# Kernel tuning notes

Hardware: AMD Instinct MI355X
Metric: run time of the kernel (lower is better)

## Reference

```python
import jax, jax.numpy as jnp
import numpy as np

N_SAMPLES = 2 ** 15  # 32768
NYQUIST = 22050.0 / 2.0
MIN_FREQ = 40.0 / NYQUIST
MAX_FREQ = 4000.0 / NYQUIST
FREQ_RANGE = MAX_FREQ - MIN_FREQ


def interp_linear(x, out_size):
    """torch F.interpolate(mode='linear', align_corners=False) along last axis."""
    in_size = x.shape[-1]
    scale = in_size / out_size
    coords = (jnp.arange(out_size, dtype=x.dtype) + 0.5) * scale - 0.5
    coords = jnp.clip(coords, 0.0, in_size - 1)
    lo = jnp.floor(coords).astype(jnp.int32)
    hi = jnp.minimum(lo + 1, in_size - 1)
    w = coords - lo.astype(x.dtype)
    return x[..., lo] * (1.0 - w) + x[..., hi] * w


def translate(pair, shift, scale):
    # angle of complex(pair[:,:,0], pair[:,:,1]) / pi, then affine
    angle = jnp.arctan2(pair[:, :, 1, :], pair[:, :, 0, :]) / np.pi
    return shift + angle * scale


def setup_inputs() -> dict:
    key = jax.random.key(0)
    k1, k2 = jax.random.split(key)
    x = jax.random.normal(k1, (16, 8, 10, 128), dtype=jnp.float32)
    noise = jax.random.normal(k2, (16, 8, N_SAMPLES), dtype=jnp.float32)
    return {"x": x, "noise": noise}


def reference(x, noise):
    # x: (batch, n_osc, 10, time_ctrl); noise: (batch, n_osc, N_SAMPLES)
    basic = x[:, :, 0:2, :]
    amp = jnp.sqrt(jnp.sum(basic * basic, axis=2))            # (b, o, t)
    amp = interp_linear(amp, N_SAMPLES)                       # (b, o, N)

    f0 = translate(basic, MIN_FREQ, FREQ_RANGE)               # control-rate
    mix = interp_linear(translate(x[:, :, 2:4, :], 1.0, 0.5), N_SAMPLES)
    harm_amp = amp * mix
    noise_amp = amp * (1.0 - mix)

    noise_std = translate(x[:, :, 4:6, :], MIN_FREQ, FREQ_RANGE)
    mod_factor = translate(x[:, :, 6:8, :], 0.25, 4.75)
    b = translate(x[:, :, 8:10, :], 0.1, 9.9)

    # band_filtered_noise: narrowband noise as a frequency-jittered sine
    f0_fr = interp_linear(f0, N_SAMPLES)
    std_fr = interp_linear(noise_std, N_SAMPLES)
    bfn = jnp.sin(jnp.cumsum(f0_fr + noise * std_fr, axis=-1))
    noise_sig = noise_amp * bfn

    mod_factor = interp_linear(mod_factor, N_SAMPLES)
    b = interp_linear(b, N_SAMPLES)
    mod = b * jnp.sin(jnp.cumsum(mod_factor, axis=-1))
    sig = harm_amp * jnp.sin(jnp.cumsum(f0_fr, axis=-1) + mod)

    mixed = noise_sig + sig                                   # (b, o, N)
    return jnp.mean(mixed, axis=1, keepdims=True)             # (b, 1, N)
```

## Files before the change

kernel.cpp:

```cpp
#include <hip/hip_runtime.h>
#include <math.h>

#define NS     32768
#define NB     128
#define CELL   16
#define CPB    32
#define PART   (CELL * CPB)
#define NPARTS (NS / PART)
#define TPB    256
#define NBATCH 16
#define GRID   (NBATCH * NPARTS)

__device__ __forceinline__ float sinr(float x) {
    return __builtin_amdgcn_sinf(x - rintf(x));
}

__device__ __forceinline__ void seg_params(int i, int& lo, int& hi,
                                           double& w0, double& wst) {
    if (i < 128)            { lo = 0;   hi = 1;   w0 = 0.0; wst = 0.0; }
    else if (i >= NS - 128) { lo = 127; hi = 127; w0 = 0.0; wst = 0.0; }
    else {
        lo = (i - 128) >> 8;  hi = lo + 1;
        int off = (i - 128) & 255;
        w0 = (off + 0.5) * (1.0 / 256.0);
        wst = 1.0 / 256.0;
    }
}

__device__ __forceinline__ double bin_value(const float* xs, int q, int j) {
    const double PI_    = 3.14159265358979323846;
    const double INV2PI = 0.15915494309189533576888376337251;
    const double MINF   = 40.0 / 11025.0;
    const double FRNG   = (4000.0 - 40.0) / 11025.0;
    if (q == 0) {
        double a0 = (double)xs[j], a1 = (double)xs[NB + j];
        return sqrt(a0 * a0 + a1 * a1);
    }
    double ang = atan2((double)xs[(2 * q - 1) * NB + j],
                       (double)xs[(2 * q - 2) * NB + j]) / PI_;
    double sh, sc;
    if      (q == 1) { sh = MINF; sc = FRNG; }
    else if (q == 2) { sh = 1.0;  sc = 0.5;  }
    else if (q == 3) { sh = MINF; sc = FRNG; }
    else if (q == 4) { sh = 0.25; sc = 4.75; }
    else             { sh = 0.1;  sc = 9.9;  }
    double v = sh + ang * sc;
    if (q != 2) v *= INV2PI;
    return v;
}

__device__ __forceinline__ void cell_totals(
        const float4* nn, double f0L, double dF0, double stL, double dSt,
        double mfL, double dMf, double w0, double wst,
        double& t1, double& t3, double& t2) {
    float4 A0 = nn[0], A1 = nn[1], A2 = nn[2], A3 = nn[3];
    float nf[CELL] = {A0.x, A0.y, A0.z, A0.w, A1.x, A1.y, A1.z, A1.w,
                      A2.x, A2.y, A2.z, A2.w, A3.x, A3.y, A3.z, A3.w};
    double S0 = 0.0, S1 = 0.0;
    #pragma unroll
    for (int j = 0; j < CELL; ++j) {
        S0 += (double)nf[j];
        S1 += (double)j * (double)nf[j];
    }
    double sw = 16.0 * w0 + 120.0 * wst;
    t3 = 16.0 * f0L + dF0 * sw;
    t2 = 16.0 * mfL + dMf * sw;
    t1 = t3 + stL * S0 + dSt * (w0 * S0 + wst * S1);
}

__global__ __launch_bounds__(TPB, 4)
void span_kernel(const float* __restrict__ xg, const float* __restrict__ ng,
                 double* __restrict__ wspan) {
    __shared__ double binsA[8][3][4];
    __shared__ double wtot[4][8][3];

    int bx = blockIdx.x, b = bx >> 6, p = bx & (NPARTS - 1);
    int tid = threadIdx.x, lane = tid & 63, wid = tid >> 6;
    int h = tid & 7, c = tid >> 3;
    int P = p * PART;
    int b0 = (P - 128) >> 8; if (b0 < 0) b0 = 0;

    int s  = (b << 3) + h;
    int i0 = P + c * CELL;
    const float4* nn = reinterpret_cast<const float4*>(ng + (size_t)s * NS + i0);

    if (tid < 96) {
        int j = tid & 3, r = (tid >> 2) % 3, h2 = tid / 12;
        int q = (r == 0) ? 1 : (r == 1) ? 3 : 4;
        const float* xs = xg + (size_t)((b << 3) + h2) * 10 * NB;
        binsA[h2][r][j] = bin_value(xs, q, min(b0 + j, NB - 1));
    }
    __syncthreads();

    int lo, hi; double w0, wst;
    seg_params(i0, lo, hi, w0, wst);
    int jL = lo - b0, jH = hi - b0;
    double f0L = binsA[h][0][jL], dF0 = binsA[h][0][jH] - f0L;
    double stL = binsA[h][1][jL], dSt = binsA[h][1][jH] - stL;
    double mfL = binsA[h][2][jL], dMf = binsA[h][2][jH] - mfL;

    double t1, t3, t2;
    cell_totals(nn, f0L, dF0, stL, dSt, mfL, dMf, w0, wst, t1, t3, t2);

    double v1 = t1, v3 = t3, v2 = t2;
    #pragma unroll
    for (int d = 8; d < 64; d <<= 1) {
        double u1 = __shfl_up(v1, d);
        double u3 = __shfl_up(v3, d);
        double u2 = __shfl_up(v2, d);
        if (lane >= d) { v1 += u1; v3 += u3; v2 += u2; }
    }
    if (lane >= 56) { wtot[wid][h][0] = v1; wtot[wid][h][1] = v3; wtot[wid][h][2] = v2; }
    __syncthreads();
    if (tid < 24) {
        int hh = tid & 7, k = tid >> 3;
        double t = wtot[0][hh][k] + wtot[1][hh][k] + wtot[2][hh][k] + wtot[3][hh][k];
        wspan[((size_t)(((b << 3) + hh) * NPARTS) + p) * 3 + k] = t;
    }
}

__global__ __launch_bounds__(TPB, 4)
void fm2_kernel(const float* __restrict__ xg, const float* __restrict__ ng,
                const double* __restrict__ wspan, float* __restrict__ out) {
    __shared__ double binsA[8][3][4];
    __shared__ float  binsB[8][6][4];
    __shared__ double wtot[4][8][3];
    __shared__ double pref[8][3];

    int bx = blockIdx.x, b = bx >> 6, p = bx & (NPARTS - 1);
    int tid = threadIdx.x, lane = tid & 63, wid = tid >> 6;
    int h = tid & 7, c = tid >> 3;
    int P = p * PART;
    int b0 = (P - 128) >> 8; if (b0 < 0) b0 = 0;

    int s  = (b << 3) + h;
    int i0 = P + c * CELL;
    const float4* nn = reinterpret_cast<const float4*>(ng + (size_t)s * NS + i0);
    float4 A0 = nn[0], A1 = nn[1], A2 = nn[2], A3 = nn[3];

    if (tid < 192) {
        int j = tid & 3, q = (tid >> 2) % 6, h2 = tid / 24;
        const float* xs = xg + (size_t)((b << 3) + h2) * 10 * NB;
        double v = bin_value(xs, q, min(b0 + j, NB - 1));
        binsB[h2][q][j] = (float)v;
        if      (q == 1) binsA[h2][0][j] = v;
        else if (q == 3) binsA[h2][1][j] = v;
        else if (q == 4) binsA[h2][2][j] = v;
    } else if (tid < 216) {
        int t2 = tid - 192, hh = t2 & 7, k = t2 >> 3;
        const double* sp = wspan + ((size_t)(((b << 3) + hh) * NPARTS)) * 3 + k;
        double acc = 0.0;
        for (int q2 = 0; q2 < p; ++q2) acc += sp[q2 * 3];
        pref[hh][k] = acc;
    }
    __syncthreads();

    int lo, hi; double w0, wst;
    seg_params(i0, lo, hi, w0, wst);
    int jL = lo - b0, jH = hi - b0;
    double f0L = binsA[h][0][jL], dF0 = binsA[h][0][jH] - f0L;
    double stL = binsA[h][1][jL], dSt = binsA[h][1][jH] - stL;
    double mfL = binsA[h][2][jL], dMf = binsA[h][2][jH] - mfL;

    double t1, t3, t2;
    cell_totals(nn, f0L, dF0, stL, dSt, mfL, dMf, w0, wst, t1, t3, t2);

    double v1 = t1, v3 = t3, v2 = t2;
    #pragma unroll
    for (int d = 8; d < 64; d <<= 1) {
        double u1 = __shfl_up(v1, d);
        double u3 = __shfl_up(v3, d);
        double u2 = __shfl_up(v2, d);
        if (lane >= d) { v1 += u1; v3 += u3; v2 += u2; }
    }
    if (lane >= 56) { wtot[wid][h][0] = v1; wtot[wid][h][1] = v3; wtot[wid][h][2] = v2; }
    __syncthreads();
    double b1 = 0.0, b3 = 0.0, b2 = 0.0;
    #pragma unroll
    for (int k = 0; k < 3; ++k)
        if (wid > k) { b1 += wtot[k][h][0]; b3 += wtot[k][h][1]; b2 += wtot[k][h][2]; }

    double a1 = pref[h][0] + b1 + (v1 - t1);
    double a3 = pref[h][1] + b3 + (v3 - t3);
    double a2 = pref[h][2] + b2 + (v2 - t2);
    float fr1 = (float)(a1 - rint(a1));
    float fr3 = (float)(a3 - rint(a3));
    float fr2 = (float)(a2 - rint(a2));

    float amL = binsB[h][0][jL], dAm = binsB[h][0][jH] - amL;
    float g0L = binsB[h][1][jL], gF0 = binsB[h][1][jH] - g0L;
    float mxL = binsB[h][2][jL], dMx = binsB[h][2][jH] - mxL;
    float gsL = binsB[h][3][jL], gSt = binsB[h][3][jH] - gsL;
    float gmL = binsB[h][4][jL], gMf = binsB[h][4][jH] - gmL;
    float bbL = binsB[h][5][jL], dBb = binsB[h][5][jH] - bbL;
    float w0f = (float)w0, wsf = (float)wst;

    float nf[CELL] = {A0.x, A0.y, A0.z, A0.w, A1.x, A1.y, A1.z, A1.w,
                      A2.x, A2.y, A2.z, A2.w, A3.x, A3.y, A3.z, A3.w};
    float arr[CELL];
    float d1 = 0.f, d2 = 0.f, d3 = 0.f;
    #pragma unroll
    for (int j = 0; j < CELL; ++j) {
        float wf  = fmaf((float)j, wsf, w0f);
        float f0v = fmaf(wf, gF0, g0L);
        float stv = fmaf(wf, gSt, gsL);
        float mfv = fmaf(wf, gMf, gmL);
        d3 += f0v;
        d1 += fmaf(nf[j], stv, f0v);
        d2 += mfv;
        float ampv = fmaf(wf, dAm, amL);
        float mixv = fmaf(wf, dMx, mxL);
        float bv   = fmaf(wf, dBb, bbL);
        float s2 = sinr(fr2 + d2);
        float s1 = sinr(fr1 + d1);
        float s3 = sinr(fmaf(bv, s2, fr3 + d3));
        float harm = ampv * mixv;
        arr[j] = fmaf(harm, s3, (ampv - harm) * s1);
    }

    #pragma unroll
    for (int m = 1; m <= 4; m <<= 1) {
        #pragma unroll
        for (int j = 0; j < CELL; ++j) arr[j] += __shfl_xor(arr[j], m);
    }
    if (h == 0) {
        float4* op = reinterpret_cast<float4*>(out + (size_t)b * NS + i0);
        #pragma unroll
        for (int j4 = 0; j4 < 4; ++j4)
            op[j4] = make_float4(arr[j4 * 4 + 0] * 0.125f, arr[j4 * 4 + 1] * 0.125f,
                                 arr[j4 * 4 + 2] * 0.125f, arr[j4 * 4 + 3] * 0.125f);
    }
}

extern "C" void kernel_launch(void* const* d_in, const int* in_sizes, int n_in,
                              void* d_out, int out_size, void* d_ws, size_t ws_size,
                              hipStream_t stream) {
    const float* x     = (const float*)d_in[0];
    const float* noise = (const float*)d_in[1];
    float* out = (float*)d_out;
    double* wspan = (double*)d_ws;
    span_kernel<<<GRID, TPB, 0, stream>>>(x, noise, wspan);
    fm2_kernel<<<GRID, TPB, 0, stream>>>(x, noise, wspan, out);
}
```

Measured before the change: 85.42 us.

## Split scan into three kernels with stored per-cell prefixes and precomputed bins

The pipeline is restructured into three stages. The first computes per-cell exclusive prefixes and per-span totals and writes both to workspace, using a 32-lane shuffle scan per oscillator so no LDS cross-wave reduction is needed. A small fix kernel then scans the span totals and precomputes every control-bin value. The final kernel reads these instead of redoing the noise summation, the serial span-prefix loop and the bin evaluation. The cost is an extra launch and extra global traffic for the per-cell doubles, about 3 MB written and read back.

```diff
diff --git a/kernel.cpp b/kernel.cpp
--- a/kernel.cpp
+++ b/kernel.cpp
@@ -10,6 +10,7 @@
 #define TPB    256
 #define NBATCH 16
 #define GRID   (NBATCH * NPARTS)
+#define NCELL  (NS / CELL)
 
 __device__ __forceinline__ float sinr(float x) {
     return __builtin_amdgcn_sinf(x - rintf(x));
@@ -68,26 +69,23 @@
     t1 = t3 + stL * S0 + dSt * (w0 * S0 + wst * S1);
 }
 
-__global__ __launch_bounds__(TPB, 4)
-void span_kernel(const float* __restrict__ xg, const float* __restrict__ ng,
-                 double* __restrict__ wspan) {
+__global__ __launch_bounds__(TPB)
+void span1_kernel(const float* __restrict__ xg, const float* __restrict__ ng,
+                  double* __restrict__ wcell, double* __restrict__ wspan) {
     __shared__ double binsA[8][3][4];
-    __shared__ double wtot[4][8][3];
-
-    int bx = blockIdx.x, b = bx >> 6, p = bx & (NPARTS - 1);
-    int tid = threadIdx.x, lane = tid & 63, wid = tid >> 6;
-    int h = tid & 7, c = tid >> 3;
+
+    int bx = blockIdx.x, bb = bx >> 6, p = bx & (NPARTS - 1);
+    int tid = threadIdx.x, lane = tid & 63;
+    int h = tid >> 5, c = tid & 31;
     int P = p * PART;
     int b0 = (P - 128) >> 8; if (b0 < 0) b0 = 0;
-
-    int s  = (b << 3) + h;
+    int s  = (bb << 3) + h;
     int i0 = P + c * CELL;
-    const float4* nn = reinterpret_cast<const float4*>(ng + (size_t)s * NS + i0);
 
     if (tid < 96) {
         int j = tid & 3, r = (tid >> 2) % 3, h2 = tid / 12;
         int q = (r == 0) ? 1 : (r == 1) ? 3 : 4;
-        const float* xs = xg + (size_t)((b << 3) + h2) * 10 * NB;
+        const float* xs = xg + (size_t)((bb << 3) + h2) * 10 * NB;
         binsA[h2][r][j] = bin_value(xs, q, min(b0 + j, NB - 1));
     }
     __syncthreads();
@@ -99,104 +97,88 @@
     double stL = binsA[h][1][jL], dSt = binsA[h][1][jH] - stL;
     double mfL = binsA[h][2][jL], dMf = binsA[h][2][jH] - mfL;
 
+    const float4* nn = reinterpret_cast<const float4*>(ng + (size_t)s * NS + i0);
     double t1, t3, t2;
     cell_totals(nn, f0L, dF0, stL, dSt, mfL, dMf, w0, wst, t1, t3, t2);
 
     double v1 = t1, v3 = t3, v2 = t2;
     #pragma unroll
-    for (int d = 8; d < 64; d <<= 1) {
+    for (int d = 1; d < 32; d <<= 1) {
         double u1 = __shfl_up(v1, d);
         double u3 = __shfl_up(v3, d);
         double u2 = __shfl_up(v2, d);
-        if (lane >= d) { v1 += u1; v3 += u3; v2 += u2; }
-    }
-    if (lane >= 56) { wtot[wid][h][0] = v1; wtot[wid][h][1] = v3; wtot[wid][h][2] = v2; }
-    __syncthreads();
-    if (tid < 24) {
-        int hh = tid & 7, k = tid >> 3;
-        double t = wtot[0][hh][k] + wtot[1][hh][k] + wtot[2][hh][k] + wtot[3][hh][k];
-        wspan[((size_t)(((b << 3) + hh) * NPARTS) + p) * 3 + k] = t;
-    }
-}
-
-__global__ __launch_bounds__(TPB, 4)
-void fm2_kernel(const float* __restrict__ xg, const float* __restrict__ ng,
-                const double* __restrict__ wspan, float* __restrict__ out) {
-    __shared__ double binsA[8][3][4];
-    __shared__ float  binsB[8][6][4];
-    __shared__ double wtot[4][8][3];
-    __shared__ double pref[8][3];
-
-    int bx = blockIdx.x, b = bx >> 6, p = bx & (NPARTS - 1);
-    int tid = threadIdx.x, lane = tid & 63, wid = tid >> 6;
+        if ((lane & 31) >= d) { v1 += u1; v3 += u3; v2 += u2; }
+    }
+
+    size_t cb = ((size_t)s * NCELL + (size_t)p * CPB + c) * 3;
+    wcell[cb + 0] = v1 - t1;
+    wcell[cb + 1] = v3 - t3;
+    wcell[cb + 2] = v2 - t2;
+    if (c == 31) {
+        size_t sb = ((size_t)s * NPARTS + p) * 3;
+        wspan[sb + 0] = v1; wspan[sb + 1] = v3; wspan[sb + 2] = v2;
+    }
+}
+
+__global__ __launch_bounds__(TPB)
+void fix_kernel(const float* __restrict__ xg, const double* __restrict__ wspan,
+                double* __restrict__ wpref, float* __restrict__ wbins) {
+    int s = blockIdx.x, tid = threadIdx.x, lane = tid & 63, wid = tid >> 6;
+    const float* xs = xg + (size_t)s * 10 * NB;
+    #pragma unroll
+    for (int r = 0; r < 3; ++r) {
+        int idx = tid + r * TPB;
+        wbins[(size_t)s * 768 + idx] = (float)bin_value(xs, idx >> 7, idx & 127);
+    }
+    if (wid < 3) {
+        int k = wid;
+        double t = wspan[((size_t)s * NPARTS + lane) * 3 + k];
+        double v = t;
+        #pragma unroll
+        for (int d = 1; d < 64; d <<= 1) {
+            double u = __shfl_up(v, d);
+            if (lane >= d) v += u;
+        }
+        wpref[((size_t)s * NPARTS + lane) * 3 + k] = v - t;
+    }
+}
+
+__global__ __launch_bounds__(TPB)
+void fm3_kernel(const float* __restrict__ ng, const double* __restrict__ wcell,
+                const double* __restrict__ wpref, const float* __restrict__ wbins,
+                float* __restrict__ out) {
+    int bx = blockIdx.x, bb = bx >> 6, p = bx & (NPARTS - 1);
+    int tid = threadIdx.x;
     int h = tid & 7, c = tid >> 3;
-    int P = p * PART;
-    int b0 = (P - 128) >> 8; if (b0 < 0) b0 = 0;
-
-    int s  = (b << 3) + h;
-    int i0 = P + c * CELL;
-    const float4* nn = reinterpret_cast<const float4*>(ng + (size_t)s * NS + i0);
-    float4 A0 = nn[0], A1 = nn[1], A2 = nn[2], A3 = nn[3];
-
-    if (tid < 192) {
-        int j = tid & 3, q = (tid >> 2) % 6, h2 = tid / 24;
-        const float* xs = xg + (size_t)((b << 3) + h2) * 10 * NB;
-        double v = bin_value(xs, q, min(b0 + j, NB - 1));
-        binsB[h2][q][j] = (float)v;
-        if      (q == 1) binsA[h2][0][j] = v;
-        else if (q == 3) binsA[h2][1][j] = v;
-        else if (q == 4) binsA[h2][2][j] = v;
-    } else if (tid < 216) {
-        int t2 = tid - 192, hh = t2 & 7, k = t2 >> 3;
-        const double* sp = wspan + ((size_t)(((b << 3) + hh) * NPARTS)) * 3 + k;
-        double acc = 0.0;
-        for (int q2 = 0; q2 < p; ++q2) acc += sp[q2 * 3];
-        pref[hh][k] = acc;
-    }
-    __syncthreads();
+    int P = p * PART, i0 = P + c * CELL;
+    int s = (bb << 3) + h;
 
     int lo, hi; double w0, wst;
     seg_params(i0, lo, hi, w0, wst);
-    int jL = lo - b0, jH = hi - b0;
-    double f0L = binsA[h][0][jL], dF0 = binsA[h][0][jH] - f0L;
-    double stL = binsA[h][1][jL], dSt = binsA[h][1][jH] - stL;
-    double mfL = binsA[h][2][jL], dMf = binsA[h][2][jH] - mfL;
-
-    double t1, t3, t2;
-    cell_totals(nn, f0L, dF0, stL, dSt, mfL, dMf, w0, wst, t1, t3, t2);
-
-    double v1 = t1, v3 = t3, v2 = t2;
-    #pragma unroll
-    for (int d = 8; d < 64; d <<= 1) {
-        double u1 = __shfl_up(v1, d);
-        double u3 = __shfl_up(v3, d);
-        double u2 = __shfl_up(v2, d);
-        if (lane >= d) { v1 += u1; v3 += u3; v2 += u2; }
-    }
-    if (lane >= 56) { wtot[wid][h][0] = v1; wtot[wid][h][1] = v3; wtot[wid][h][2] = v2; }
-    __syncthreads();
-    double b1 = 0.0, b3 = 0.0, b2 = 0.0;
-    #pragma unroll
-    for (int k = 0; k < 3; ++k)
-        if (wid > k) { b1 += wtot[k][h][0]; b3 += wtot[k][h][1]; b2 += wtot[k][h][2]; }
-
-    double a1 = pref[h][0] + b1 + (v1 - t1);
-    double a3 = pref[h][1] + b3 + (v3 - t3);
-    double a2 = pref[h][2] + b2 + (v2 - t2);
+
+    size_t cb = ((size_t)s * NCELL + (size_t)p * CPB + c) * 3;
+    size_t pb = ((size_t)s * NPARTS + p) * 3;
+    double a1 = wcell[cb + 0] + wpref[pb + 0];
+    double a3 = wcell[cb + 1] + wpref[pb + 1];
+    double a2 = wcell[cb + 2] + wpref[pb + 2];
     float fr1 = (float)(a1 - rint(a1));
     float fr3 = (float)(a3 - rint(a3));
     float fr2 = (float)(a2 - rint(a2));
 
-    float amL = binsB[h][0][jL], dAm = binsB[h][0][jH] - amL;
-    float g0L = binsB[h][1][jL], gF0 = binsB[h][1][jH] - g0L;
-    float mxL = binsB[h][2][jL], dMx = binsB[h][2][jH] - mxL;
-    float gsL = binsB[h][3][jL], gSt = binsB[h][3][jH] - gsL;
-    float gmL = binsB[h][4][jL], gMf = binsB[h][4][jH] - gmL;
-    float bbL = binsB[h][5][jL], dBb = binsB[h][5][jH] - bbL;
+    const float* B = wbins + (size_t)s * 768;
+    float amL = B[lo],       dAm = B[hi] - amL;
+    float g0L = B[128 + lo], gF0 = B[128 + hi] - g0L;
+    float mxL = B[256 + lo], dMx = B[256 + hi] - mxL;
+    float gsL = B[384 + lo], gSt = B[384 + hi] - gsL;
+    float gmL = B[512 + lo], gMf = B[512 + hi] - gmL;
+    float bbL = B[640 + lo], dBb = B[640 + hi] - bbL;
     float w0f = (float)w0, wsf = (float)wst;
 
+    const float4* nn = reinterpret_cast<const float4*>(ng + (size_t)s * NS + i0);
+    float4 A0 = nn[0], A1 = nn[1], A2 = nn[2], A3 = nn[3];
     float nf[CELL] = {A0.x, A0.y, A0.z, A0.w, A1.x, A1.y, A1.z, A1.w,
                       A2.x, A2.y, A2.z, A2.w, A3.x, A3.y, A3.z, A3.w};
+
     float arr[CELL];
     float d1 = 0.f, d2 = 0.f, d3 = 0.f;
     #pragma unroll
@@ -224,7 +206,7 @@
         for (int j = 0; j < CELL; ++j) arr[j] += __shfl_xor(arr[j], m);
     }
     if (h == 0) {
-        float4* op = reinterpret_cast<float4*>(out + (size_t)b * NS + i0);
+        float4* op = reinterpret_cast<float4*>(out + (size_t)bb * NS + i0);
         #pragma unroll
         for (int j4 = 0; j4 < 4; ++j4)
             op[j4] = make_float4(arr[j4 * 4 + 0] * 0.125f, arr[j4 * 4 + 1] * 0.125f,
@@ -238,7 +220,11 @@
     const float* x     = (const float*)d_in[0];
     const float* noise = (const float*)d_in[1];
     float* out = (float*)d_out;
-    double* wspan = (double*)d_ws;
-    span_kernel<<<GRID, TPB, 0, stream>>>(x, noise, wspan);
-    fm2_kernel<<<GRID, TPB, 0, stream>>>(x, noise, wspan, out);
-}
+    double* wcell = (double*)d_ws;
+    double* wspan = wcell + (size_t)128 * NCELL * 3;
+    double* wpref = wspan + (size_t)128 * NPARTS * 3;
+    float*  wbins = (float*)(wpref + (size_t)128 * NPARTS * 3);
+    span1_kernel<<<GRID, TPB, 0, stream>>>(x, noise, wcell, wspan);
+    fix_kernel<<<128, TPB, 0, stream>>>(x, wspan, wpref, wbins);
+    fm3_kernel<<<GRID, TPB, 0, stream>>>(noise, wcell, wpref, wbins, out);
+}
```

Result: faster. 81.58 us (-4.5%).

## Fuse span and synthesis kernels into one cooperative kernel with grid sync

Applied to the files above, without the earlier changes.

Merges the two-pass scan (span totals, then synthesis) into a single cooperative kernel that publishes per-block partial sums, calls grid.sync, then builds prefixes and synthesizes the output. Cell size doubles to 32 samples per thread, halving the grid to 512 blocks so all blocks can be co-resident, and the cross-block prefix is now summed in parallel by 8 lanes per entry. Noise is read once per pass per element, and the second launch and the recomputation of bins and local scans are removed. The cost is a grid-wide barrier, fewer and heavier threads with higher register pressure (launch bounds lowered to 2), and reliance on cooperative-launch residency.

```diff
diff --git a/kernel.cpp b/kernel.cpp
--- a/kernel.cpp
+++ b/kernel.cpp
@@ -1,15 +1,19 @@
 #include <hip/hip_runtime.h>
+#include <hip/hip_cooperative_groups.h>
 #include <math.h>
+
+namespace cg = cooperative_groups;
 
 #define NS     32768
 #define NB     128
-#define CELL   16
+#define CELL   32
 #define CPB    32
 #define PART   (CELL * CPB)
 #define NPARTS (NS / PART)
 #define TPB    256
 #define NBATCH 16
 #define GRID   (NBATCH * NPARTS)
+#define NBIN   6
 
 __device__ __forceinline__ float sinr(float x) {
     return __builtin_amdgcn_sinf(x - rintf(x));
@@ -49,58 +53,58 @@
     return v;
 }
 
-__device__ __forceinline__ void cell_totals(
-        const float4* nn, double f0L, double dF0, double stL, double dSt,
-        double mfL, double dMf, double w0, double wst,
-        double& t1, double& t3, double& t2) {
-    float4 A0 = nn[0], A1 = nn[1], A2 = nn[2], A3 = nn[3];
-    float nf[CELL] = {A0.x, A0.y, A0.z, A0.w, A1.x, A1.y, A1.z, A1.w,
-                      A2.x, A2.y, A2.z, A2.w, A3.x, A3.y, A3.z, A3.w};
-    double S0 = 0.0, S1 = 0.0;
-    #pragma unroll
-    for (int j = 0; j < CELL; ++j) {
-        S0 += (double)nf[j];
-        S1 += (double)j * (double)nf[j];
-    }
-    double sw = 16.0 * w0 + 120.0 * wst;
-    t3 = 16.0 * f0L + dF0 * sw;
-    t2 = 16.0 * mfL + dMf * sw;
-    t1 = t3 + stL * S0 + dSt * (w0 * S0 + wst * S1);
-}
-
-__global__ __launch_bounds__(TPB, 4)
-void span_kernel(const float* __restrict__ xg, const float* __restrict__ ng,
-                 double* __restrict__ wspan) {
-    __shared__ double binsA[8][3][4];
+__global__ __launch_bounds__(TPB, 2)
+void fm_all_kernel(const float* __restrict__ xg, const float* __restrict__ ng,
+                   double* __restrict__ wspan, float* __restrict__ out) {
+    cg::grid_group grid = cg::this_grid();
+
+    __shared__ double binsA[8][3][NBIN];
+    __shared__ float  binsB[8][6][NBIN];
     __shared__ double wtot[4][8][3];
-
-    int bx = blockIdx.x, b = bx >> 6, p = bx & (NPARTS - 1);
+    __shared__ double prefL[8][3];
+
+    int bx = blockIdx.x, bb = bx >> 5, p = bx & (NPARTS - 1);
     int tid = threadIdx.x, lane = tid & 63, wid = tid >> 6;
     int h = tid & 7, c = tid >> 3;
     int P = p * PART;
     int b0 = (P - 128) >> 8; if (b0 < 0) b0 = 0;
-
-    int s  = (b << 3) + h;
+    int s  = (bb << 3) + h;
     int i0 = P + c * CELL;
-    const float4* nn = reinterpret_cast<const float4*>(ng + (size_t)s * NS + i0);
-
-    if (tid < 96) {
-        int j = tid & 3, r = (tid >> 2) % 3, h2 = tid / 12;
-        int q = (r == 0) ? 1 : (r == 1) ? 3 : 4;
-        const float* xs = xg + (size_t)((b << 3) + h2) * 10 * NB;
-        binsA[h2][r][j] = bin_value(xs, q, min(b0 + j, NB - 1));
+
+    for (int idx = tid; idx < 8 * 6 * NBIN; idx += TPB) {
+        int j = idx % NBIN, q = (idx / NBIN) % 6, h2 = idx / (6 * NBIN);
+        const float* xs = xg + (size_t)((bb << 3) + h2) * 10 * NB;
+        double v = bin_value(xs, q, min(b0 + j, NB - 1));
+        binsB[h2][q][j] = (float)v;
+        if      (q == 1) binsA[h2][0][j] = v;
+        else if (q == 3) binsA[h2][1][j] = v;
+        else if (q == 4) binsA[h2][2][j] = v;
     }
     __syncthreads();
 
     int lo, hi; double w0, wst;
     seg_params(i0, lo, hi, w0, wst);
     int jL = lo - b0, jH = hi - b0;
+
     double f0L = binsA[h][0][jL], dF0 = binsA[h][0][jH] - f0L;
     double stL = binsA[h][1][jL], dSt = binsA[h][1][jH] - stL;
     double mfL = binsA[h][2][jL], dMf = binsA[h][2][jH] - mfL;
 
-    double t1, t3, t2;
-    cell_totals(nn, f0L, dF0, stL, dSt, mfL, dMf, w0, wst, t1, t3, t2);
+    const float4* nn = reinterpret_cast<const float4*>(ng + (size_t)s * NS + i0);
+    double S0 = 0.0, S1 = 0.0;
+    #pragma unroll
+    for (int q4 = 0; q4 < CELL / 4; ++q4) {
+        float4 nv = nn[q4];
+        double jd = (double)(q4 * 4);
+        S0 += (double)nv.x; S1 += jd * (double)nv.x;
+        S0 += (double)nv.y; S1 += (jd + 1.0) * (double)nv.y;
+        S0 += (double)nv.z; S1 += (jd + 2.0) * (double)nv.z;
+        S0 += (double)nv.w; S1 += (jd + 3.0) * (double)nv.w;
+    }
+    double sw = 32.0 * w0 + 496.0 * wst;
+    double t3 = 32.0 * f0L + dF0 * sw;
+    double t2 = 32.0 * mfL + dMf * sw;
+    double t1 = t3 + stL * S0 + dSt * (w0 * S0 + wst * S1);
 
     double v1 = t1, v3 = t3, v2 = t2;
     #pragma unroll
@@ -112,77 +116,34 @@
     }
     if (lane >= 56) { wtot[wid][h][0] = v1; wtot[wid][h][1] = v3; wtot[wid][h][2] = v2; }
     __syncthreads();
-    if (tid < 24) {
-        int hh = tid & 7, k = tid >> 3;
-        double t = wtot[0][hh][k] + wtot[1][hh][k] + wtot[2][hh][k] + wtot[3][hh][k];
-        wspan[((size_t)(((b << 3) + hh) * NPARTS) + p) * 3 + k] = t;
-    }
-}
-
-__global__ __launch_bounds__(TPB, 4)
-void fm2_kernel(const float* __restrict__ xg, const float* __restrict__ ng,
-                const double* __restrict__ wspan, float* __restrict__ out) {
-    __shared__ double binsA[8][3][4];
-    __shared__ float  binsB[8][6][4];
-    __shared__ double wtot[4][8][3];
-    __shared__ double pref[8][3];
-
-    int bx = blockIdx.x, b = bx >> 6, p = bx & (NPARTS - 1);
-    int tid = threadIdx.x, lane = tid & 63, wid = tid >> 6;
-    int h = tid & 7, c = tid >> 3;
-    int P = p * PART;
-    int b0 = (P - 128) >> 8; if (b0 < 0) b0 = 0;
-
-    int s  = (b << 3) + h;
-    int i0 = P + c * CELL;
-    const float4* nn = reinterpret_cast<const float4*>(ng + (size_t)s * NS + i0);
-    float4 A0 = nn[0], A1 = nn[1], A2 = nn[2], A3 = nn[3];
-
-    if (tid < 192) {
-        int j = tid & 3, q = (tid >> 2) % 6, h2 = tid / 24;
-        const float* xs = xg + (size_t)((b << 3) + h2) * 10 * NB;
-        double v = bin_value(xs, q, min(b0 + j, NB - 1));
-        binsB[h2][q][j] = (float)v;
-        if      (q == 1) binsA[h2][0][j] = v;
-        else if (q == 3) binsA[h2][1][j] = v;
-        else if (q == 4) binsA[h2][2][j] = v;
-    } else if (tid < 216) {
-        int t2 = tid - 192, hh = t2 & 7, k = t2 >> 3;
-        const double* sp = wspan + ((size_t)(((b << 3) + hh) * NPARTS)) * 3 + k;
-        double acc = 0.0;
-        for (int q2 = 0; q2 < p; ++q2) acc += sp[q2 * 3];
-        pref[hh][k] = acc;
-    }
-    __syncthreads();
-
-    int lo, hi; double w0, wst;
-    seg_params(i0, lo, hi, w0, wst);
-    int jL = lo - b0, jH = hi - b0;
-    double f0L = binsA[h][0][jL], dF0 = binsA[h][0][jH] - f0L;
-    double stL = binsA[h][1][jL], dSt = binsA[h][1][jH] - stL;
-    double mfL = binsA[h][2][jL], dMf = binsA[h][2][jH] - mfL;
-
-    double t1, t3, t2;
-    cell_totals(nn, f0L, dF0, stL, dSt, mfL, dMf, w0, wst, t1, t3, t2);
-
-    double v1 = t1, v3 = t3, v2 = t2;
-    #pragma unroll
-    for (int d = 8; d < 64; d <<= 1) {
-        double u1 = __shfl_up(v1, d);
-        double u3 = __shfl_up(v3, d);
-        double u2 = __shfl_up(v2, d);
-        if (lane >= d) { v1 += u1; v3 += u3; v2 += u2; }
-    }
-    if (lane >= 56) { wtot[wid][h][0] = v1; wtot[wid][h][1] = v3; wtot[wid][h][2] = v2; }
-    __syncthreads();
     double b1 = 0.0, b3 = 0.0, b2 = 0.0;
     #pragma unroll
     for (int k = 0; k < 3; ++k)
         if (wid > k) { b1 += wtot[k][h][0]; b3 += wtot[k][h][1]; b2 += wtot[k][h][2]; }
 
-    double a1 = pref[h][0] + b1 + (v1 - t1);
-    double a3 = pref[h][1] + b3 + (v3 - t3);
-    double a2 = pref[h][2] + b2 + (v2 - t2);
+    double e1 = b1 + v1 - t1, e3 = b3 + v3 - t3, e2 = b2 + v2 - t2;
+
+    if (tid >= 248) {
+        size_t sb = ((size_t)s * NPARTS + p) * 3;
+        wspan[sb + 0] = b1 + v1; wspan[sb + 1] = b3 + v3; wspan[sb + 2] = b2 + v2;
+    }
+
+    grid.sync();
+
+    if (tid < 192) {
+        int r = tid & 7, g = tid >> 3, k = g % 3, h2 = g / 3;
+        const double* sp = wspan + ((size_t)(((bb << 3) + h2) * NPARTS)) * 3 + k;
+        double acc = 0.0;
+        for (int q = r; q < p; q += 8) acc += sp[q * 3];
+        #pragma unroll
+        for (int m = 1; m <= 4; m <<= 1) acc += __shfl_xor(acc, m);
+        if (r == 0) { prefL[h2][k] = acc; }
+    }
+    __syncthreads();
+
+    double a1 = e1 + prefL[h][0];
+    double a3 = e3 + prefL[h][1];
+    double a2 = e2 + prefL[h][2];
     float fr1 = (float)(a1 - rint(a1));
     float fr3 = (float)(a3 - rint(a3));
     float fr2 = (float)(a2 - rint(a2));
@@ -195,27 +156,31 @@
     float bbL = binsB[h][5][jL], dBb = binsB[h][5][jH] - bbL;
     float w0f = (float)w0, wsf = (float)wst;
 
-    float nf[CELL] = {A0.x, A0.y, A0.z, A0.w, A1.x, A1.y, A1.z, A1.w,
-                      A2.x, A2.y, A2.z, A2.w, A3.x, A3.y, A3.z, A3.w};
     float arr[CELL];
     float d1 = 0.f, d2 = 0.f, d3 = 0.f;
     #pragma unroll
-    for (int j = 0; j < CELL; ++j) {
-        float wf  = fmaf((float)j, wsf, w0f);
-        float f0v = fmaf(wf, gF0, g0L);
-        float stv = fmaf(wf, gSt, gsL);
-        float mfv = fmaf(wf, gMf, gmL);
-        d3 += f0v;
-        d1 += fmaf(nf[j], stv, f0v);
-        d2 += mfv;
-        float ampv = fmaf(wf, dAm, amL);
-        float mixv = fmaf(wf, dMx, mxL);
-        float bv   = fmaf(wf, dBb, bbL);
-        float s2 = sinr(fr2 + d2);
-        float s1 = sinr(fr1 + d1);
-        float s3 = sinr(fmaf(bv, s2, fr3 + d3));
-        float harm = ampv * mixv;
-        arr[j] = fmaf(harm, s3, (ampv - harm) * s1);
+    for (int q4 = 0; q4 < CELL / 4; ++q4) {
+        float4 nv = nn[q4];
+        float nf[4] = {nv.x, nv.y, nv.z, nv.w};
+        #pragma unroll
+        for (int u = 0; u < 4; ++u) {
+            int j = q4 * 4 + u;
+            float wf  = fmaf((float)j, wsf, w0f);
+            float f0v = fmaf(wf, gF0, g0L);
+            float stv = fmaf(wf, gSt, gsL);
+            float mfv = fmaf(wf, gMf, gmL);
+            d3 += f0v;
+            d1 += fmaf(nf[u], stv, f0v);
+            d2 += mfv;
+            float ampv = fmaf(wf, dAm, amL);
+            float mixv = fmaf(wf, dMx, mxL);
+            float bv   = fmaf(wf, dBb, bbL);
+            float s2 = sinr(fr2 + d2);
+            float s1 = sinr(fr1 + d1);
+            float s3 = sinr(fmaf(bv, s2, fr3 + d3));
+            float harm = ampv * mixv;
+            arr[j] = fmaf(harm, s3, (ampv - harm) * s1);
+        }
     }
 
     #pragma unroll
@@ -224,9 +189,9 @@
         for (int j = 0; j < CELL; ++j) arr[j] += __shfl_xor(arr[j], m);
     }
     if (h == 0) {
-        float4* op = reinterpret_cast<float4*>(out + (size_t)b * NS + i0);
-        #pragma unroll
-        for (int j4 = 0; j4 < 4; ++j4)
+        float4* op = reinterpret_cast<float4*>(out + (size_t)bb * NS + i0);
+        #pragma unroll
+        for (int j4 = 0; j4 < CELL / 4; ++j4)
             op[j4] = make_float4(arr[j4 * 4 + 0] * 0.125f, arr[j4 * 4 + 1] * 0.125f,
                                  arr[j4 * 4 + 2] * 0.125f, arr[j4 * 4 + 3] * 0.125f);
     }
@@ -239,6 +204,8 @@
     const float* noise = (const float*)d_in[1];
     float* out = (float*)d_out;
     double* wspan = (double*)d_ws;
-    span_kernel<<<GRID, TPB, 0, stream>>>(x, noise, wspan);
-    fm2_kernel<<<GRID, TPB, 0, stream>>>(x, noise, wspan, out);
-}
+
+    void* args[] = {(void*)&x, (void*)&noise, (void*)&wspan, (void*)&out};
+    hipLaunchCooperativeKernel((const void*)fm_all_kernel, dim3(GRID), dim3(TPB),
+                               args, 0, stream);
+}
```

New measurement: 139.8 us. 1.64x slower.
